# Optimization experiments

Measured on AMD Instinct MI355X. Metric: run time of the kernel, lower is better.

## Reference

```python
import jax, jax.numpy as jnp
import numpy as np
from jax import lax

BATCH = 512
NUM_ITER = 5
NUM_CLASSES = 10
NUM_PRIMARY = 32 * 6 * 6  # 1152
CAPS_IN = 8
CAPS_OUT = 16
EPS = 1e-5


def _bn(x, g, b):
    # training-mode batchnorm over (N,H,W) per channel, NCHW
    m = x.mean(axis=(0, 2, 3), keepdims=True)
    v = x.var(axis=(0, 2, 3), keepdims=True)
    return g[None, :, None, None] * (x - m) * lax.rsqrt(v + EPS) + b[None, :, None, None]


def _conv(x, w, b, stride):
    y = lax.conv_general_dilated(x, w, (stride, stride), 'VALID',
                                 dimension_numbers=('NCHW', 'OIHW', 'NCHW'))
    return y + b[None, :, None, None]


def _squash(s):
    # per source: n / (n^2 + 1) * x
    n = jnp.linalg.norm(s, axis=-1, keepdims=True)
    return n / (n * n + 1.0) * s


def setup_inputs() -> dict:
    key = jax.random.key(0)
    ks = jax.random.split(key, 10)
    d = {
        'x': jax.random.normal(ks[0], (BATCH, 1, 28, 28), jnp.float32),
        'conv1_w': jax.random.normal(ks[1], (256, 1, 9, 9), jnp.float32) * 0.05,
        'conv1_b': jnp.zeros((256,), jnp.float32),
        'bn1_g': jnp.ones((256,), jnp.float32),
        'bn1_b': jnp.zeros((256,), jnp.float32),
        # 8 branch convs of (32,256,9,9) stacked into one (256,256,9,9) conv
        'conv2_w': jax.random.normal(ks[2], (256, 256, 9, 9), jnp.float32) * 0.01,
        'conv2_b': jnp.zeros((256,), jnp.float32),
        'bn2_g': jnp.ones((256,), jnp.float32),
        'bn2_b': jnp.zeros((256,), jnp.float32),
        'W': jax.random.normal(ks[3], (NUM_CLASSES, NUM_PRIMARY, CAPS_IN, CAPS_OUT), jnp.float32),
    }
    return d


def reference(x, conv1_w, conv1_b, bn1_g, bn1_b, conv2_w, conv2_b, bn2_g, bn2_b, W):
    B = x.shape[0]
    # input conv: (B,1,28,28) -> (B,256,20,20)
    y = jax.nn.relu(_bn(_conv(x, conv1_w, conv1_b, 1), bn1_g, bn1_b))
    # primary caps conv (8 branches fused): (B,256,6,6)
    z = jax.nn.relu(_bn(_conv(y, conv2_w, conv2_b, 2), bn2_g, bn2_b))
    # capsules: (B,8,32,6,6) -> (B, 1152, 8); capsule dim = branch index
    u = z.reshape(B, CAPS_IN, NUM_PRIMARY).transpose(0, 2, 1)
    # prediction vectors u_hat: (B, 10, 1152, 16)
    u_hat = jnp.einsum('bid,jide->bjie', u, W)

    def routing_step(b_log, _):
        c = jax.nn.softmax(b_log, axis=1)              # over 10 output caps
        s = jnp.einsum('bji,bjie->bje', c, u_hat)      # (B,10,16)
        v = _squash(s)
        b_log = b_log + jnp.einsum('bjie,bje->bji', u_hat, v)
        return b_log, v

    b0 = jnp.zeros((B, NUM_CLASSES, NUM_PRIMARY), u_hat.dtype)
    _, vs = lax.scan(routing_step, b0, None, length=NUM_ITER)
    return vs[-1]  # (B, 10, 16)
```

## Files before the change

### kernel.cpp

```cpp
#include <hip/hip_runtime.h>

typedef unsigned short u16;
typedef unsigned int   u32;
typedef __attribute__((ext_vector_type(8))) short bf16x8;
typedef __attribute__((ext_vector_type(4))) float f32x4;

__device__ __forceinline__ float bf2f(u16 u) { return __uint_as_float(((u32)u) << 16); }
__device__ __forceinline__ float bflo(u32 u) { return __uint_as_float(u << 16); }
__device__ __forceinline__ float bfhi(u32 u) { return __uint_as_float(u & 0xffff0000u); }
__device__ __forceinline__ u16 f2bf(float f) {
    u32 x = __float_as_uint(f);
    x += 0x7fffu + ((x >> 16) & 1u);
    return (u16)(x >> 16);
}
__device__ __forceinline__ u16 f2h(float f) {
    _Float16 h = (_Float16)f;
    return __builtin_bit_cast(u16, h);
}
__device__ __forceinline__ float h2f(u16 u) {
    return (float)__builtin_bit_cast(_Float16, u);
}

__global__ __launch_bounds__(256) void repack_w2_kernel(const float* __restrict__ w2,
                                                        u16* __restrict__ w2r) {
    int idx = blockIdx.x * 256 + threadIdx.x;
    int cil = idx & 31;
    int co  = (idx >> 5) & 255;
    int ccc = (idx >> 13) & 7;
    int kk  = idx >> 16;
    int ci  = ccc * 32 + cil;
    w2r[idx] = f2bf(w2[(size_t)co * 20736 + (size_t)ci * 81 + kk]);
}

__global__ __launch_bounds__(256) void repack_W_kernel(const float* __restrict__ W,
                                                       float* __restrict__ Wt2) {
    int idx = blockIdx.x * 256 + threadIdx.x;
    int d  = idx & 7;
    int je = (idx >> 3) % 160;
    int i  = idx / 1280;
    int j = je >> 4, e = je & 15;
    Wt2[idx] = W[(((size_t)j * 1152 + i) * 8 + d) * 16 + e];
}

__global__ __launch_bounds__(256) void conv1_kernel(const float* __restrict__ x,
                                                    const float* __restrict__ w1,
                                                    const float* __restrict__ b1,
                                                    u16* __restrict__ y,
                                                    float* __restrict__ sum1,
                                                    float* __restrict__ sumsq1) {
    __shared__ float xs[784];
    const int b = blockIdx.x;
    const int t = threadIdx.x;
    const float* xb = x + (size_t)b * 784;
    for (int idx = t; idx < 784; idx += 256) xs[idx] = xb[idx];
    float w[81];
#pragma unroll
    for (int q = 0; q < 81; ++q) w[q] = w1[(size_t)t * 81 + q];
    const float bias = b1[t];
    __syncthreads();

    float sl = 0.f, ssl = 0.f;
    u16* yb = y + (size_t)b * 400 * 256 + t;
    for (int oh = 0; oh < 20; ++oh) {
        float acc[20];
#pragma unroll
        for (int ow = 0; ow < 20; ++ow) acc[ow] = bias;
#pragma unroll
        for (int kh = 0; kh < 9; ++kh) {
            const float4* rp = (const float4*)(&xs[(oh + kh) * 28]);
            float r[28];
#pragma unroll
            for (int k4 = 0; k4 < 7; ++k4) {
                float4 f = rp[k4];
                r[k4 * 4 + 0] = f.x; r[k4 * 4 + 1] = f.y;
                r[k4 * 4 + 2] = f.z; r[k4 * 4 + 3] = f.w;
            }
#pragma unroll
            for (int kw = 0; kw < 9; ++kw) {
                const float wv = w[kh * 9 + kw];
#pragma unroll
                for (int ow = 0; ow < 20; ++ow)
                    acc[ow] = fmaf(wv, r[ow + kw], acc[ow]);
            }
        }
#pragma unroll
        for (int ow = 0; ow < 20; ++ow) {
            u16 q = f2bf(acc[ow]);
            float rv = bf2f(q);
            sl += rv; ssl += rv * rv;
            yb[(size_t)(oh * 20 + ow) * 256] = q;
        }
    }
    atomicAdd(&sum1[t], sl);
    atomicAdd(&sumsq1[t], ssl);
}

__global__ void finalize_bn_kernel(const float* __restrict__ sum,
                                   const float* __restrict__ sumsq,
                                   const float* __restrict__ gam,
                                   const float* __restrict__ bet,
                                   float* __restrict__ scale,
                                   float* __restrict__ shift, float inv_n) {
    int c = threadIdx.x;
    float m = sum[c] * inv_n;
    float var = sumsq[c] * inv_n - m * m;
    float sc = gam[c] * rsqrtf(var + 1e-5f);
    scale[c] = sc;
    shift[c] = bet[c] - m * sc;
}

__global__ __launch_bounds__(256) void bnpack_kernel(u32* __restrict__ y32,
                                                     const float* __restrict__ scale1,
                                                     const float* __restrict__ shift1) {
    const int b = blockIdx.x;
    const int t = threadIdx.x;
    const int c2 = (t & 127) * 2;
    const float s0 = scale1[c2],     s1 = scale1[c2 + 1];
    const float h0 = shift1[c2],     h1 = shift1[c2 + 1];
    u32* base = y32 + (size_t)b * 51200;
    for (int q = 0; q < 200; ++q) {
        const int idx = t + q * 256;
        u32 v = base[idx];
        float a = fmaxf(0.f, fmaf(s0, bflo(v), h0));
        float c = fmaxf(0.f, fmaf(s1, bfhi(v), h1));
        base[idx] = (u32)f2bf(a) | ((u32)f2bf(c) << 16);
    }
}

__global__ __launch_bounds__(256, 2) void conv2_mfma_kernel(const u16* __restrict__ y,
                                                            const u16* __restrict__ w2r,
                                                            const float* __restrict__ b2,
                                                            float* __restrict__ z_raw,
                                                            float* __restrict__ sum2,
                                                            float* __restrict__ sumsq2) {
    __shared__ __align__(16) u16 stg[240 * 136];
    const int g  = blockIdx.x >> 1;
    const int cb = (blockIdx.x & 1) * 128;
    const int b0 = g * 2;
    const int t = threadIdx.x;
    const int wave = t >> 6, lane = t & 63;
    const int n16 = lane & 15, quad = lane >> 4;
    const int img = wave & 1, c64 = wave >> 1;

    f32x4 zero = {0.f, 0.f, 0.f, 0.f};
    f32x4 acc[4][3];
#pragma unroll
    for (int ct = 0; ct < 4; ++ct)
#pragma unroll
        for (int pt = 0; pt < 3; ++pt) acc[ct][pt] = zero;

    int brow[3];
#pragma unroll
    for (int pt = 0; pt < 3; ++pt) {
        int pos = pt * 16 + n16; if (pos > 35) pos = 35;
        const int oh = (pos * 43) >> 8;
        const int ow = pos - oh * 6;
        brow[pt] = (img * 6 + oh) * 20 + 2 * ow;
    }

    const int laneoff = (cb + c64 * 64 + n16) * 32 + quad * 8;

    bf16x8 abuf[3][4];
    bf16x8 bbuf[2][3];

    auto loadA = [&](bf16x8 (&dst)[4], const u16* basep, int ittv) {
        const u16* wa = basep + (ittv >> 2) * 65536 + (ittv & 3) * 8192;
#pragma unroll
        for (int ct = 0; ct < 4; ++ct)
            dst[ct] = *((const bf16x8*)(wa + ct * 512));
    };
    auto loadB = [&](bf16x8 (&dst)[3], int ittv) {
        const int kw = ittv >> 2, ccc = ittv & 3;
#pragma unroll
        for (int pt = 0; pt < 3; ++pt)
            dst[pt] = *((const bf16x8*)(stg + (brow[pt] + kw) * 136
                                        + ccc * 32 + quad * 8));
    };

    {
        const u16* w0 = w2r + laneoff;
        loadA(abuf[0], w0, 0);
        loadA(abuf[1], w0, 1);
        loadA(abuf[2], w0, 2);
    }

    for (int kh = 0; kh < 9; ++kh) {
        for (int cp = 0; cp < 2; ++cp) {
            __syncthreads();
#pragma unroll
            for (int q = 0; q < 15; ++q) {
                const int v = t + q * 256;
                const int rI = v >> 4, c16 = v & 15;
                const int i2 = (rI >= 120) ? 1 : 0;
                const int rr = rI - i2 * 120;
                const int oh = rr / 20;
                const int iw = rr - oh * 20;
                const int ip = (2 * oh + kh) * 20 + iw;
                const uint4 d = *((const uint4*)(y + ((size_t)(b0 + i2) * 400 + ip) * 256
                                                 + cp * 128 + c16 * 8));
                *((uint4*)(stg + rI * 136 + c16 * 8)) = d;
            }
            __syncthreads();

            const int khn = (cp == 1) ? kh + 1 : kh;
            const int cpn = cp ^ 1;
            const u16* wbase = w2r + (size_t)kh * 589824 + (size_t)cp * 32768 + laneoff;
            const u16* wnext = w2r + (size_t)khn * 589824 + (size_t)cpn * 32768 + laneoff;

            loadB(bbuf[0], 0);
            loadB(bbuf[1], 1);

#pragma unroll
            for (int itt = 0; itt < 36; ++itt) {
                const int a_i = itt % 3, b_i = itt % 2;
#pragma unroll
                for (int ct = 0; ct < 4; ++ct)
#pragma unroll
                    for (int pt = 0; pt < 3; ++pt)
                        acc[ct][pt] = __builtin_amdgcn_mfma_f32_16x16x32_bf16(
                            abuf[a_i][ct], bbuf[b_i][pt], acc[ct][pt], 0, 0, 0);
                if (itt < 33) loadA(abuf[a_i], wbase, itt + 3);
                else          loadA(abuf[a_i], wnext, itt + 3 - 36);
                if (itt < 34) loadB(bbuf[b_i], itt + 2);
            }
        }
    }

#pragma unroll
    for (int ct = 0; ct < 4; ++ct) {
#pragma unroll
        for (int r = 0; r < 4; ++r) {
            const int co = cb + c64 * 64 + ct * 16 + quad * 4 + r;
            const float bias = b2[co];
            float s = 0.f, ss = 0.f;
#pragma unroll
            for (int pt = 0; pt < 3; ++pt) {
                const int pos = pt * 16 + n16;
                if (pos < 36) {
                    float v = acc[ct][pt][r] + bias;
                    z_raw[((size_t)(b0 + img) * 256 + co) * 36 + pos] = v;
                    s += v; ss += v * v;
                }
            }
#pragma unroll
            for (int m = 1; m < 16; m <<= 1) {
                s  += __shfl_xor(s,  m, 64);
                ss += __shfl_xor(ss, m, 64);
            }
            if (n16 == 0) { atomicAdd(&sum2[co], s); atomicAdd(&sumsq2[co], ss); }
        }
    }
}

__global__ __launch_bounds__(256) void ubuild_kernel(const float* __restrict__ z_raw,
                                                     const float* __restrict__ scale2,
                                                     const float* __restrict__ shift2,
                                                     u16* __restrict__ ut16) {
    const int b = blockIdx.x;
    const int t = threadIdx.x;
    const int d = t >> 5, m = t & 31;
    const float sc = scale2[t], sh = shift2[t];
    const float* zp = z_raw + ((size_t)b * 256 + t) * 36;
    u32* up = (u32*)(ut16 + ((size_t)b * 8 + d) * 1152 + m * 36);
#pragma unroll
    for (int q = 0; q < 18; ++q) {
        float v0 = fmaxf(0.f, fmaf(sc, zp[2 * q],     sh));
        float v1 = fmaxf(0.f, fmaf(sc, zp[2 * q + 1], sh));
        up[q] = (u32)f2h(v0) | ((u32)f2h(v1) << 16);
    }
}

__global__ __launch_bounds__(256) void uhat_kernel(const u16* __restrict__ ut16,
                                                   const float* __restrict__ Wt2,
                                                   u16* __restrict__ u_hat,
                                                   float* __restrict__ s0g) {
    __shared__ float utl[8 * 8 * 144];
    const int bg = blockIdx.x >> 3;
    const int ic = blockIdx.x & 7;
    const int b0 = bg * 8, i0 = ic * 144;
    for (int v = threadIdx.x; v < 8 * 8 * 144; v += 256) {
        int ii = v % 144; int d = (v / 144) & 7; int bb = v / 1152;
        utl[v] = h2f(ut16[(size_t)(b0 + bb) * 9216 + d * 1152 + i0 + ii]);
    }
    __syncthreads();
    for (int q = 0; q < 90; ++q) {
        int o = q * 256 + threadIdx.x;
        int ii = o / 160, je = o - ii * 160;
        const float* wp = Wt2 + ((size_t)(i0 + ii) * 160 + je) * 8;
        float w[8];
#pragma unroll
        for (int d = 0; d < 8; ++d) w[d] = wp[d];
#pragma unroll
        for (int bb = 0; bb < 8; ++bb) {
            float acc = 0.f;
#pragma unroll
            for (int d = 0; d < 8; ++d) acc = fmaf(w[d], utl[bb * 1152 + d * 144 + ii], acc);
            u_hat[(size_t)(b0 + bb) * 184320 + (size_t)(i0 + ii) * 160 + je] = f2h(acc);
        }
    }
    __syncthreads();
#pragma unroll
    for (int p = 0; p < 5; ++p) {
        const int pair = p * 256 + threadIdx.x;
        const int bb = pair / 160, je = pair - (pair / 160) * 160;
        const u16* up = u_hat + (size_t)(b0 + bb) * 184320 + (size_t)i0 * 160 + je;
        float s = 0.f;
        for (int ii = 0; ii < 144; ++ii) s += h2f(up[(size_t)ii * 160]);
        atomicAdd(&s0g[(size_t)(b0 + bb) * 160 + je], s);
    }
}

__global__ __launch_bounds__(384) void routing_kernel(const u16* __restrict__ u_hat,
                                                      const float* __restrict__ s0g,
                                                      float* __restrict__ out) {
    __shared__ __align__(16) u16 uhs[2][96 * 168];
    __shared__ float cl[10 * 96];
    __shared__ float part[320];
    __shared__ float sv[160];
    __shared__ float bls[12 * 96 * 11];
    const int t = threadIdx.x;
    const int b = blockIdx.x;
    const u16* uh = u_hat + (size_t)b * 184320;
    const int hB = (t < 320) ? (t / 160) : 0;
    const int je = (t < 320) ? (t - hB * 160) : 0;
    const int jB = je >> 4;

    uint4 rg[5];
    {
        const u16* src = uh;
#pragma unroll
        for (int q = 0; q < 5; ++q) {
            int v = t + q * 384, r = v / 20, c16 = v - r * 20;
            rg[q] = *((const uint4*)(src + r * 160 + c16 * 8));
        }
    }
    for (int v = t; v < 12 * 96 * 11; v += 384) bls[v] = 0.f;
    if (t < 160) sv[t] = 0.1f * s0g[(size_t)b * 160 + t];
    __syncthreads();
    if (t < 10) {
        float n2 = 0.f;
#pragma unroll
        for (int e2 = 0; e2 < 16; ++e2) { float xx = sv[t * 16 + e2]; n2 += xx * xx; }
        float n = sqrtf(n2);
        float f = n / (n2 + 1.f);
#pragma unroll
        for (int e2 = 0; e2 < 16; ++e2) sv[t * 16 + e2] *= f;
    }
#pragma unroll
    for (int q = 0; q < 5; ++q) {
        int v = t + q * 384, r = v / 20, c16 = v - r * 20;
        *((uint4*)(&uhs[0][r * 168 + c16 * 8])) = rg[q];
    }

    for (int k = 1; k <= 4; ++k) {
        float b0a = 0.f, b1a = 0.f, b2a = 0.f, b3a = 0.f;
        for (int c = 0; c < 12; ++c) {
            const int p = c & 1;
            const bool last = (k == 4) && (c == 11);
            __syncthreads();
            if (!last) {
                const int nc = (c == 11) ? 0 : c + 1;
                const u16* src = uh + (size_t)nc * 15360;
#pragma unroll
                for (int q = 0; q < 5; ++q) {
                    int v = t + q * 384, r = v / 20, c16 = v - r * 20;
                    rg[q] = *((const uint4*)(src + r * 160 + c16 * 8));
                }
            }
            if (t < 96) {
                const u16* row = uhs[p] + t * 168;
                float* blrow = &bls[(c * 96 + t) * 11];
                float bj[10];
#pragma unroll
                for (int j = 0; j < 10; ++j) {
                    uint4 a = *((const uint4*)(row + j * 16));
                    uint4 bq = *((const uint4*)(row + j * 16 + 8));
                    const float* vv = &sv[j * 16];
                    float dj = h2f((u16)(a.x & 0xffff)) * vv[0]  + h2f((u16)(a.x >> 16)) * vv[1]
                             + h2f((u16)(a.y & 0xffff)) * vv[2]  + h2f((u16)(a.y >> 16)) * vv[3]
                             + h2f((u16)(a.z & 0xffff)) * vv[4]  + h2f((u16)(a.z >> 16)) * vv[5]
                             + h2f((u16)(a.w & 0xffff)) * vv[6]  + h2f((u16)(a.w >> 16)) * vv[7]
                             + h2f((u16)(bq.x & 0xffff)) * vv[8]  + h2f((u16)(bq.x >> 16)) * vv[9]
                             + h2f((u16)(bq.y & 0xffff)) * vv[10] + h2f((u16)(bq.y >> 16)) * vv[11]
                             + h2f((u16)(bq.z & 0xffff)) * vv[12] + h2f((u16)(bq.z >> 16)) * vv[13]
                             + h2f((u16)(bq.w & 0xffff)) * vv[14] + h2f((u16)(bq.w >> 16)) * vv[15];
                    float nb = blrow[j] + dj;
                    blrow[j] = nb;
                    bj[j] = nb;
                }
                float mx = bj[0];
#pragma unroll
                for (int j = 1; j < 10; ++j) mx = fmaxf(mx, bj[j]);
                float s = 0.f;
#pragma unroll
                for (int j = 0; j < 10; ++j) { bj[j] = __expf(bj[j] - mx); s += bj[j]; }
                float inv = 1.f / s;
#pragma unroll
                for (int j = 0; j < 10; ++j) cl[j * 96 + t] = bj[j] * inv;
            }
            __syncthreads();
            if (t < 320) {
                const int r0 = hB * 48;
                const float* clj = &cl[jB * 96 + r0];
                const u16* up = uhs[p] + r0 * 168 + je;
#pragma unroll 3
                for (int il = 0; il < 48; il += 4) {
                    b0a = fmaf(clj[il],     h2f(up[(il)     * 168]), b0a);
                    b1a = fmaf(clj[il + 1], h2f(up[(il + 1) * 168]), b1a);
                    b2a = fmaf(clj[il + 2], h2f(up[(il + 2) * 168]), b2a);
                    b3a = fmaf(clj[il + 3], h2f(up[(il + 3) * 168]), b3a);
                }
            }
            if (!last) {
#pragma unroll
                for (int q = 0; q < 5; ++q) {
                    int v = t + q * 384, r = v / 20, c16 = v - r * 20;
                    *((uint4*)(&uhs[p ^ 1][r * 168 + c16 * 8])) = rg[q];
                }
            }
        }
        __syncthreads();
        if (t < 320) part[t] = (b0a + b1a) + (b2a + b3a);
        __syncthreads();
        if (t < 160) sv[t] = part[t] + part[t + 160];
        __syncthreads();
        if (t < 10) {
            float n2 = 0.f;
#pragma unroll
            for (int e2 = 0; e2 < 16; ++e2) { float xx = sv[t * 16 + e2]; n2 += xx * xx; }
            float n = sqrtf(n2);
            float f = n / (n2 + 1.f);
#pragma unroll
            for (int e2 = 0; e2 < 16; ++e2) sv[t * 16 + e2] *= f;
        }
    }
    __syncthreads();
    if (t < 160) out[(size_t)b * 160 + t] = sv[t];
}

extern "C" void kernel_launch(void* const* d_in, const int* in_sizes, int n_in,
                              void* d_out, int out_size, void* d_ws, size_t ws_size,
                              hipStream_t stream) {
    const float* x   = (const float*)d_in[0];
    const float* w1  = (const float*)d_in[1];
    const float* b1  = (const float*)d_in[2];
    const float* g1  = (const float*)d_in[3];
    const float* be1 = (const float*)d_in[4];
    const float* w2  = (const float*)d_in[5];
    const float* b2  = (const float*)d_in[6];
    const float* g2  = (const float*)d_in[7];
    const float* be2 = (const float*)d_in[8];
    const float* W   = (const float*)d_in[9];
    float* out = (float*)d_out;

    const size_t OFF_UHAT = 8192;
    const size_t OFF_Y    = 8192;
    const size_t OFF_W2R  = 104865792ull;
    const size_t OFF_Z    = 126099456ull;
    const size_t OFF_UT   = 188751872ull;
    const size_t OFF_S0   = 198189056ull;
    const size_t OFF_WT   = 207626240ull;
    const size_t WS_NEED  = 213524480ull;
    if (ws_size < WS_NEED) return;

    char* ws = (char*)d_ws;
    float* sum1   = (float*)(ws + 0);
    float* sumsq1 = (float*)(ws + 1024);
    float* sum2   = (float*)(ws + 2048);
    float* sumsq2 = (float*)(ws + 3072);
    float* scale1 = (float*)(ws + 4096);
    float* shift1 = (float*)(ws + 5120);
    float* scale2 = (float*)(ws + 6144);
    float* shift2 = (float*)(ws + 7168);
    u16*   y     = (u16*)(ws + OFF_Y);
    u16*   w2r   = (u16*)(ws + OFF_W2R);
    float* z_raw = (float*)(ws + OFF_Z);
    u16*   ut16  = (u16*)(ws + OFF_UT);
    float* s0g   = (float*)(ws + OFF_S0);
    float* Wt2   = (float*)(ws + OFF_WT);
    u16*   u_hat = (u16*)(ws + OFF_UHAT);

    hipMemsetAsync(ws, 0, 4096, stream);
    hipMemsetAsync(ws + OFF_S0, 0, 327680, stream);

    hipLaunchKernelGGL(repack_w2_kernel, dim3(20736), dim3(256), 0, stream, w2, w2r);
    hipLaunchKernelGGL(repack_W_kernel,  dim3(5760),  dim3(256), 0, stream, W, Wt2);
    hipLaunchKernelGGL(conv1_kernel,     dim3(512),   dim3(256), 0, stream,
                       x, w1, b1, y, sum1, sumsq1);
    hipLaunchKernelGGL(finalize_bn_kernel, dim3(1), dim3(256), 0, stream,
                       sum1, sumsq1, g1, be1, scale1, shift1, 1.f / 204800.f);
    hipLaunchKernelGGL(bnpack_kernel,    dim3(512),   dim3(256), 0, stream,
                       (u32*)y, scale1, shift1);
    hipLaunchKernelGGL(conv2_mfma_kernel, dim3(512),  dim3(256), 0, stream,
                       y, w2r, b2, z_raw, sum2, sumsq2);
    hipLaunchKernelGGL(finalize_bn_kernel, dim3(1), dim3(256), 0, stream,
                       sum2, sumsq2, g2, be2, scale2, shift2, 1.f / 18432.f);
    hipLaunchKernelGGL(ubuild_kernel,    dim3(512),   dim3(256), 0, stream,
                       z_raw, scale2, shift2, ut16);
    hipLaunchKernelGGL(uhat_kernel,      dim3(512),   dim3(256), 0, stream,
                       ut16, Wt2, u_hat, s0g);
    hipLaunchKernelGGL(routing_kernel,   dim3(512),   dim3(384), 0, stream,
                       u_hat, s0g, out);
}
```

Measured before the change: 1.016 ms.

## Reuse staged input rows across kernel rows via parity-ordered ring buffer in conv2

Reorders the conv2 kernel-row loop into even/odd parity groups so consecutive kh steps share most input rows in LDS. Only the one new input row per step is loaded into a circular slot; previously all 6 rows were restaged for every kh. This cuts global-to-LDS staging traffic for the y tensor by roughly 5x. In exchange it adds modular slot index math and requires the weight pointer sequence to follow the new order.

Result: slower. 1.064 ms (+4.7%).

```diff
diff --git a/kernel.cpp b/kernel.cpp
--- a/kernel.cpp
+++ b/kernel.cpp
@@ -149,13 +149,12 @@
 #pragma unroll
         for (int pt = 0; pt < 3; ++pt) acc[ct][pt] = zero;
 
-    int brow[3];
+    int ohp[3], owp[3];
 #pragma unroll
     for (int pt = 0; pt < 3; ++pt) {
         int pos = pt * 16 + n16; if (pos > 35) pos = 35;
-        const int oh = (pos * 43) >> 8;
-        const int ow = pos - oh * 6;
-        brow[pt] = (img * 6 + oh) * 20 + 2 * ow;
+        ohp[pt] = (pos * 43) >> 8;
+        owp[pt] = pos - ohp[pt] * 6;
     }
 
     const int laneoff = (cb + c64 * 64 + n16) * 32 + quad * 8;
@@ -163,18 +162,21 @@
     bf16x8 abuf[3][4];
     bf16x8 bbuf[2][3];
 
+    auto wptr = [&](int st_) -> const u16* {
+        int cp_, par_, s_;
+        if (st_ < 5)       { cp_ = 0; par_ = 0; s_ = st_; }
+        else if (st_ < 9)  { cp_ = 0; par_ = 1; s_ = st_ - 5; }
+        else if (st_ < 14) { cp_ = 1; par_ = 0; s_ = st_ - 9; }
+        else               { cp_ = 1; par_ = 1; s_ = st_ - 14; }
+        const int kh_ = par_ + 2 * s_;
+        return w2r + (size_t)kh_ * 589824 + (size_t)cp_ * 32768 + laneoff;
+    };
+
     auto loadA = [&](bf16x8 (&dst)[4], const u16* basep, int ittv) {
         const u16* wa = basep + (ittv >> 2) * 65536 + (ittv & 3) * 8192;
 #pragma unroll
         for (int ct = 0; ct < 4; ++ct)
             dst[ct] = *((const bf16x8*)(wa + ct * 512));
-    };
-    auto loadB = [&](bf16x8 (&dst)[3], int ittv) {
-        const int kw = ittv >> 2, ccc = ittv & 3;
-#pragma unroll
-        for (int pt = 0; pt < 3; ++pt)
-            dst[pt] = *((const bf16x8*)(stg + (brow[pt] + kw) * 136
-                                        + ccc * 32 + quad * 8));
     };
 
     {
@@ -184,45 +186,78 @@
         loadA(abuf[2], w0, 2);
     }
 
-    for (int kh = 0; kh < 9; ++kh) {
-        for (int cp = 0; cp < 2; ++cp) {
-            __syncthreads();
+    for (int st = 0; st < 18; ++st) {
+        int cp, parity, s;
+        if (st < 5)       { cp = 0; parity = 0; s = st; }
+        else if (st < 9)  { cp = 0; parity = 1; s = st - 5; }
+        else if (st < 14) { cp = 1; parity = 0; s = st - 9; }
+        else              { cp = 1; parity = 1; s = st - 14; }
+
+        __syncthreads();
+        if (s == 0) {
 #pragma unroll
             for (int q = 0; q < 15; ++q) {
                 const int v = t + q * 256;
                 const int rI = v >> 4, c16 = v & 15;
                 const int i2 = (rI >= 120) ? 1 : 0;
                 const int rr = rI - i2 * 120;
-                const int oh = rr / 20;
-                const int iw = rr - oh * 20;
-                const int ip = (2 * oh + kh) * 20 + iw;
-                const uint4 d = *((const uint4*)(y + ((size_t)(b0 + i2) * 400 + ip) * 256
+                const int slot = rr / 20;
+                const int iw = rr - slot * 20;
+                const int ir = parity + 2 * slot;
+                const uint4 d = *((const uint4*)(y + ((size_t)(b0 + i2) * 400 + ir * 20 + iw) * 256
                                                  + cp * 128 + c16 * 8));
                 *((uint4*)(stg + rI * 136 + c16 * 8)) = d;
             }
-            __syncthreads();
-
-            const int khn = (cp == 1) ? kh + 1 : kh;
-            const int cpn = cp ^ 1;
-            const u16* wbase = w2r + (size_t)kh * 589824 + (size_t)cp * 32768 + laneoff;
-            const u16* wnext = w2r + (size_t)khn * 589824 + (size_t)cpn * 32768 + laneoff;
-
-            loadB(bbuf[0], 0);
-            loadB(bbuf[1], 1);
-
-#pragma unroll
-            for (int itt = 0; itt < 36; ++itt) {
-                const int a_i = itt % 3, b_i = itt % 2;
-#pragma unroll
-                for (int ct = 0; ct < 4; ++ct)
-#pragma unroll
-                    for (int pt = 0; pt < 3; ++pt)
-                        acc[ct][pt] = __builtin_amdgcn_mfma_f32_16x16x32_bf16(
-                            abuf[a_i][ct], bbuf[b_i][pt], acc[ct][pt], 0, 0, 0);
-                if (itt < 33) loadA(abuf[a_i], wbase, itt + 3);
-                else          loadA(abuf[a_i], wnext, itt + 3 - 36);
-                if (itt < 34) loadB(bbuf[b_i], itt + 2);
-            }
+        } else {
+            const int ir = parity + 2 * (s + 5);
+            const int slotn = (s - 1) % 6;
+#pragma unroll
+            for (int q = 0; q < 3; ++q) {
+                if (q < 2 || t < 128) {
+                    const int v = t + q * 256;
+                    const int rI = v >> 4, c16 = v & 15;
+                    const int i2 = (rI >= 20) ? 1 : 0;
+                    const int iw = rI - i2 * 20;
+                    const uint4 d = *((const uint4*)(y + ((size_t)(b0 + i2) * 400 + ir * 20 + iw) * 256
+                                                     + cp * 128 + c16 * 8));
+                    *((uint4*)(stg + ((i2 * 6 + slotn) * 20 + iw) * 136 + c16 * 8)) = d;
+                }
+            }
+        }
+        __syncthreads();
+
+        int brow[3];
+#pragma unroll
+        for (int pt = 0; pt < 3; ++pt) {
+            int slot = s + ohp[pt]; if (slot >= 6) slot -= 6;
+            brow[pt] = (img * 6 + slot) * 20 + 2 * owp[pt];
+        }
+        auto loadB = [&](bf16x8 (&dst)[3], int ittv) {
+            const int kw = ittv >> 2, ccc = ittv & 3;
+#pragma unroll
+            for (int pt = 0; pt < 3; ++pt)
+                dst[pt] = *((const bf16x8*)(stg + (brow[pt] + kw) * 136
+                                            + ccc * 32 + quad * 8));
+        };
+
+        const u16* wbase = wptr(st);
+        const u16* wnext = wptr((st < 17) ? st + 1 : st);
+
+        loadB(bbuf[0], 0);
+        loadB(bbuf[1], 1);
+
+#pragma unroll
+        for (int itt = 0; itt < 36; ++itt) {
+            const int a_i = itt % 3, b_i = itt % 2;
+#pragma unroll
+            for (int ct = 0; ct < 4; ++ct)
+#pragma unroll
+                for (int pt = 0; pt < 3; ++pt)
+                    acc[ct][pt] = __builtin_amdgcn_mfma_f32_16x16x32_bf16(
+                        abuf[a_i][ct], bbuf[b_i][pt], acc[ct][pt], 0, 0, 0);
+            if (itt < 33) loadA(abuf[a_i], wbase, itt + 3);
+            else          loadA(abuf[a_i], wnext, itt + 3 - 36);
+            if (itt < 34) loadB(bbuf[b_i], itt + 2);
         }
     }
 
```
